# Optimization experiments

Measured on AMD Instinct MI355X. Metric: run time of the kernel, lower is better.

The kernel has to match this reference:

```python
import jax, jax.numpy as jnp
import numpy as np

DIM = 2048
N_HEADS = 16
N_KV_HEADS = 8
HEAD_DIM = DIM // N_HEADS  # 128
B, S = 4, 2048
EPS = 1e-6


def _xavier_uniform(key, shape):
    fan_out, fan_in = shape
    bound = float(np.sqrt(6.0 / (fan_in + fan_out)))
    return jax.random.uniform(key, shape, jnp.float32, -bound, bound)


def _rmsnorm(x, w):
    # x: [..., head_dim]
    return x * jax.lax.rsqrt(jnp.mean(x * x, axis=-1, keepdims=True) + EPS) * w


def _apply_rope(x, cos, sin):
    # x: [B,S,H,D]; cos/sin: [B,S,D//2]; pairs (even, odd) form complex numbers
    x2 = x.reshape(*x.shape[:-1], HEAD_DIM // 2, 2)
    xr, xi = x2[..., 0], x2[..., 1]
    c = cos[:, :, None, :]
    s = sin[:, :, None, :]
    out_r = xr * c - xi * s
    out_i = xr * s + xi * c
    return jnp.stack([out_r, out_i], axis=-1).reshape(x.shape)


def setup_inputs() -> dict:
    key = jax.random.key(0)
    k1, k2, k3 = jax.random.split(key, 3)
    x = jax.random.normal(k1, (B, S, DIM), jnp.float32)
    x_mask = jnp.ones((B, S), jnp.bool_)
    # rotary frequencies (llama-style)
    inv_freq = 1.0 / (10000.0 ** (np.arange(0, HEAD_DIM, 2, dtype=np.float32) / HEAD_DIM))
    angles = np.arange(S, dtype=np.float32)[:, None] * inv_freq[None, :]  # [S, D/2]
    freqs_cos = jnp.broadcast_to(jnp.asarray(np.cos(angles)), (B, S, HEAD_DIM // 2))
    freqs_sin = jnp.broadcast_to(jnp.asarray(np.sin(angles)), (B, S, HEAD_DIM // 2))
    qkv_out = (N_HEADS + 2 * N_KV_HEADS) * HEAD_DIM
    Wqkv = _xavier_uniform(k2, (qkv_out, DIM))
    Wout = _xavier_uniform(k3, (DIM, N_HEADS * HEAD_DIM))
    qn_w = jnp.ones((HEAD_DIM,), jnp.float32)
    kn_w = jnp.ones((HEAD_DIM,), jnp.float32)
    return {"x": x, "x_mask": x_mask, "freqs_cos": freqs_cos, "freqs_sin": freqs_sin,
            "Wqkv": Wqkv, "Wout": Wout, "qn_w": qn_w, "kn_w": kn_w}


def reference(x, x_mask, freqs_cos, freqs_sin, Wqkv, Wout, qn_w, kn_w):
    bsz, seqlen, _ = x.shape
    n_rep = N_HEADS // N_KV_HEADS
    qkv = x @ Wqkv.T  # [B,S,(H+2*KV)*D]
    q_sz = N_HEADS * HEAD_DIM
    kv_sz = N_KV_HEADS * HEAD_DIM
    xq = qkv[..., :q_sz].reshape(bsz, seqlen, N_HEADS, HEAD_DIM)
    xk = qkv[..., q_sz:q_sz + kv_sz].reshape(bsz, seqlen, N_KV_HEADS, HEAD_DIM)
    xv = qkv[..., q_sz + kv_sz:].reshape(bsz, seqlen, N_KV_HEADS, HEAD_DIM)
    xq = _rmsnorm(xq, qn_w)
    xk = _rmsnorm(xk, kn_w)
    xq = _apply_rope(xq, freqs_cos, freqs_sin)
    xk = _apply_rope(xk, freqs_cos, freqs_sin)
    # GQA: repeat kv heads contiguously (matches unsqueeze(3).repeat.flatten(2,3))
    xk = jnp.repeat(xk, n_rep, axis=2)  # [B,S,H,D]
    xv = jnp.repeat(xv, n_rep, axis=2)
    scale = float(np.sqrt(1.0 / HEAD_DIM))
    scores = jnp.einsum('bqhd,bkhd->bhqk', xq, xk) * scale  # [B,H,S,S]
    mask = x_mask[:, None, None, :]  # [B,1,1,S] key mask
    scores = jnp.where(mask, scores, jnp.asarray(-1e30, scores.dtype))
    attn = jax.nn.softmax(scores, axis=-1)
    out = jnp.einsum('bhqk,bkhd->bqhd', attn, xv)  # [B,S,H,D]
    out = out.reshape(bsz, seqlen, N_HEADS * HEAD_DIM)
    return out @ Wout.T
```

## Files before the change

### kernel.cpp

```cpp
#include <hip/hip_runtime.h>

typedef unsigned short u16;
typedef unsigned int   u32;
typedef __bf16  bf16x8 __attribute__((ext_vector_type(8)));
typedef float   f32x4  __attribute__((ext_vector_type(4)));
typedef u16     u16x8  __attribute__((ext_vector_type(8)));

#define DEV __device__ __forceinline__

DEV u16 f2bf(float f) {
  u32 u = __builtin_bit_cast(u32, f);
  u += 0x7fffu + ((u >> 16) & 1u);
  return (u16)(u >> 16);
}
DEV float bf2f(u16 h) { return __builtin_bit_cast(float, (u32)h << 16); }

DEV void gl2lds16(const void* g, void* l) {
  __builtin_amdgcn_global_load_lds(
      (const __attribute__((address_space(1))) u32*)g,
      (__attribute__((address_space(3))) u32*)l, 16, 0, 0);
}

DEV f32x4 mfma16(u16x8 a, u16x8 b, f32x4 c) {
  return __builtin_amdgcn_mfma_f32_16x16x32_bf16(
      __builtin_bit_cast(bf16x8, a), __builtin_bit_cast(bf16x8, b), c, 0, 0, 0);
}

__global__ __launch_bounds__(256) void k_cast(const float* __restrict__ in,
                                              u16* __restrict__ out, long n) {
  long i = ((long)blockIdx.x * 256 + threadIdx.x) * 8;
  if (i >= n) return;
  float4 a = *(const float4*)(in + i);
  float4 b = *(const float4*)(in + i + 4);
  u16x8 o;
  o[0]=f2bf(a.x); o[1]=f2bf(a.y); o[2]=f2bf(a.z); o[3]=f2bf(a.w);
  o[4]=f2bf(b.x); o[5]=f2bf(b.y); o[6]=f2bf(b.z); o[7]=f2bf(b.w);
  *(u16x8*)(out + i) = o;
}

template<bool F32OUT>
__global__ __launch_bounds__(512, 2) void k_gemm256(
    const u16* __restrict__ A, const u16* __restrict__ B,
    u16* __restrict__ Cb, float* __restrict__ Cf, int N, int K, int nbx)
{
  __shared__ __align__(16) u16 As2[2][16384];
  __shared__ __align__(16) u16 Bs2[2][16384];

  const int per = gridDim.x >> 3;
  const int wg  = (blockIdx.x & 7) * per + (blockIdx.x >> 3);
  const int by  = wg / nbx, bx = wg - by * nbx;
  const long m0 = (long)by * 256, n0 = (long)bx * 256;

  const int tid = threadIdx.x, wv = tid >> 6, lane = tid & 63;
  const int lr = lane & 15, lg = lane >> 4;
  const int wr = wv >> 2, wc = wv & 3;

  const int r8  = tid >> 3;
  const int u   = tid & 7;
  const int kux = ((u ^ (r8 & 7)) << 3);

  const int aoffb = wr * 8192 + lr * 64;
  const int boffb = (wc >> 1) * 8192 + (wc & 1) * 4096 + lr * 64;
  const int sw0 = ((lg ^ (lr & 7)) << 3);
  const int sw1 = (((4 + lg) ^ (lr & 7)) << 3);

  f32x4 acc[8][4] = {};

  auto stageK = [&](int d, int k0) {
#pragma unroll
    for (int h = 0; h < 2; ++h) {
      const u16* ga = A + (m0 + h * 128 + r8) * (long)K + k0 + kux;
      const u16* gb = B + (n0 + h * 128 + r8) * (long)K + k0 + kux;
      gl2lds16(ga,                 &As2[d][h * 8192 + tid * 8]);
      gl2lds16(ga + 64 * (long)K,  &As2[d][h * 8192 + 4096 + tid * 8]);
      gl2lds16(gb,                 &Bs2[d][h * 8192 + tid * 8]);
      gl2lds16(gb + 64 * (long)K,  &Bs2[d][h * 8192 + 4096 + tid * 8]);
    }
  };

  const int T = K >> 6;
  stageK(0, 0);
  stageK(1, 64);

  for (int t = 0; t < T; ++t) {
    const int d = t & 1;
    if (t < T - 1) asm volatile("s_waitcnt vmcnt(8)" ::: "memory");
    else           asm volatile("s_waitcnt vmcnt(0)" ::: "memory");
    asm volatile("s_barrier" ::: "memory");

#pragma unroll
    for (int kk = 0; kk < 2; ++kk) {
      const int sw = kk ? sw1 : sw0;
      u16x8 bfrag[4];
#pragma unroll
      for (int g = 0; g < 4; ++g)
        bfrag[g] = *(const u16x8*)(&Bs2[d][boffb + g * 1024 + sw]);
#pragma unroll
      for (int mh = 0; mh < 2; ++mh) {
        u16x8 afrag[4];
#pragma unroll
        for (int j = 0; j < 4; ++j)
          afrag[j] = *(const u16x8*)(&As2[d][aoffb + (mh * 4 + j) * 1024 + sw]);
        asm volatile("s_barrier" ::: "memory");
        __builtin_amdgcn_s_setprio(1);
#pragma unroll
        for (int j = 0; j < 4; ++j)
#pragma unroll
          for (int g = 0; g < 4; ++g)
            acc[mh * 4 + j][g] = mfma16(afrag[j], bfrag[g], acc[mh * 4 + j][g]);
        __builtin_amdgcn_s_setprio(0);
        asm volatile("s_barrier" ::: "memory");
      }
    }
    __builtin_amdgcn_sched_barrier(0);
    if (t + 2 < T) stageK(d, (t + 2) << 6);
  }

#pragma unroll
  for (int f = 0; f < 8; ++f)
#pragma unroll
    for (int g = 0; g < 4; ++g)
#pragma unroll
      for (int r = 0; r < 4; ++r) {
        long row = m0 + wr * 128 + f * 16 + lg * 4 + r;
        long col = n0 + wc * 64 + g * 16 + lr;
        if (F32OUT) Cf[row * N + col] = acc[f][g][r];
        else        Cb[row * N + col] = f2bf(acc[f][g][r]);
      }
}

__global__ __launch_bounds__(256) void k_normrope(
    const u16* __restrict__ qkv, const float* __restrict__ fc,
    const float* __restrict__ fs, const float* __restrict__ qn,
    const float* __restrict__ kn,
    u16* __restrict__ Qg, u16* __restrict__ Kg)
{
  const int m = blockIdx.x;
  const int b = m >> 11, s = m & 2047;
  const int wave = threadIdx.x >> 6, lane = threadIdx.x & 63;
  const u16* row = qkv + (long)m * 4096;
  const float c  = fc[(long)m * 64 + lane];
  const float sn = fs[(long)m * 64 + lane];
  const float w0q = qn[lane * 2], w1q = qn[lane * 2 + 1];
  const float w0k = kn[lane * 2], w1k = kn[lane * 2 + 1];
  const float QS = 0.12751744f;

  for (int slot = wave; slot < 24; slot += 4) {
    u32 pair = *(const u32*)(row + slot * 128 + lane * 2);
    float x0 = bf2f((u16)(pair & 0xffffu));
    float x1 = bf2f((u16)(pair >> 16));
    float ss = x0 * x0 + x1 * x1;
#pragma unroll
    for (int msk = 1; msk < 64; msk <<= 1) ss += __shfl_xor(ss, msk, 64);
    float rms = rsqrtf(ss * (1.0f / 128.0f) + 1e-6f);
    bool isq = slot < 16;
    float w0 = isq ? w0q : w0k;
    float w1 = isq ? w1q : w1k;
    float xr = x0 * rms * w0;
    float xi = x1 * rms * w1;
    float o0 = xr * c - xi * sn;
    float o1 = xr * sn + xi * c;
    if (isq) { o0 *= QS; o1 *= QS; }
    u32 outp = (u32)f2bf(o0) | ((u32)f2bf(o1) << 16);
    if (isq)
      *(u32*)(Qg + ((long)((b * 16 + slot) * 2048 + s)) * 128 + lane * 2) = outp;
    else
      *(u32*)(Kg + ((long)((b * 8 + slot - 16) * 2048 + s)) * 128 + lane * 2) = outp;
  }
}

__global__ __launch_bounds__(256) void k_vtrans(const u16* __restrict__ qkv,
                                                u16* __restrict__ Vt)
{
  __shared__ __align__(16) u16 Ls[128 * 128];
  const int st = blockIdx.x;
  const int bk = blockIdx.y;
  const int b = bk >> 3, kvh = bk & 7;
  const int t = threadIdx.x;
  const int s0 = st * 128;
  const u16* src = qkv + ((long)(b * 2048 + s0)) * 4096 + (24 + kvh) * 128;
#pragma unroll
  for (int i = 0; i < 8; ++i) {
    int gi = i * 2048 + t * 8;
    int sl = gi >> 7, d = gi & 127;
    u16x8 v = *(const u16x8*)(src + (long)sl * 4096 + d);
    int sw = ((sl ^ (sl >> 3)) & 7) << 3;
    *(u16x8*)(&Ls[sl * 128 + (d ^ sw)]) = v;
  }
  __syncthreads();
  u16* dst = Vt + ((long)bk * 128) * 2048 + s0;
#pragma unroll
  for (int i = 0; i < 8; ++i) {
    int d = i * 16 + (t >> 4);
    int sl0 = (t & 15) * 8;
    u16x8 o;
#pragma unroll
    for (int j = 0; j < 8; ++j) {
      int sl = sl0 + j;
      int sw = ((sl ^ (sl >> 3)) & 7) << 3;
      o[j] = Ls[sl * 128 + (d ^ sw)];
    }
    *(u16x8*)(dst + (long)d * 2048 + sl0) = o;
  }
}

__global__ __launch_bounds__(256, 2) void k_attn(
    const u16* __restrict__ Qg, const u16* __restrict__ Kg,
    const u16* __restrict__ Vt, u16* __restrict__ Og)
{
  __shared__ __align__(16) u16 Kl[2 * 64 * 128];
  __shared__ __align__(16) u16 Vl[2 * 128 * 64];
  __shared__ __align__(16) u16 Pl[4][32 * 32];

  const int f   = blockIdx.x;
  const int xcd = f & 7;
  const int s8  = f >> 3;
  const int b   = s8 >> 5;
  const int kvh = xcd;
  const int mem = s8 & 31;
  const int h   = kvh * 2 + (mem & 1);
  const int qblk= mem >> 1;

  const u16*  Qp = Qg + (long)(b * 16 + h) * 2048 * 128;
  const char* Kp = (const char*)(Kg + (long)(b * 8 + kvh) * 2048 * 128);
  const char* Vp = (const char*)(Vt + (long)(b * 8 + kvh) * 128 * 2048);

  const int tid = threadIdx.x, wave = tid >> 6, lane = tid & 63;
  const int lr = lane & 15, lg = lane >> 4;
  const int q0 = qblk * 128 + wave * 32;

  u16x8 qf[2][4];
#pragma unroll
  for (int ah = 0; ah < 2; ++ah)
#pragma unroll
    for (int kk = 0; kk < 4; ++kk)
      qf[ah][kk] = *(const u16x8*)(Qp + (long)(q0 + ah * 16 + lr) * 128 + kk * 32 + lg * 8);

  f32x4 oacc[2][8] = {};
  float lsum[2][4] = {};

  int koff[4], voff[4];
#pragma unroll
  for (int i = 0; i < 4; ++i) {
    int L = i * 4096 + tid * 16;
    int key = L >> 8;
    koff[i] = key * 256 + ((L & 255) ^ ((key & 7) << 4));
    int d = L >> 7;
    voff[i] = d * 4096 + ((L & 127) ^ ((d & 7) << 4));
  }
  char* Klb = (char*)Kl;
  char* Vlb = (char*)Vl;
  u16* Pw = &Pl[wave][0];

  auto stage = [&](int sel, int k0) {
#pragma unroll
    for (int i = 0; i < 4; ++i) {
      int L = i * 4096 + tid * 16;
      gl2lds16(Kp + (long)k0 * 256 + koff[i], Klb + sel * 16384 + L);
      gl2lds16(Vp + (long)k0 * 2   + voff[i], Vlb + sel * 16384 + L);
    }
  };

  stage(0, 0);

  int cur = 0;
  for (int t = 0; t < 32; ++t) {
    if (t < 31) {
      stage(cur ^ 1, (t + 1) * 64);
      asm volatile("s_waitcnt vmcnt(8)" ::: "memory");
    } else {
      asm volatile("s_waitcnt vmcnt(0)" ::: "memory");
    }
    asm volatile("s_barrier" ::: "memory");
    const u16* Kb = Kl + cur * 8192;
    const u16* Vb = Vl + cur * 8192;

#pragma unroll
    for (int h32 = 0; h32 < 2; ++h32) {
      f32x4 sf[2][2] = {};
      __builtin_amdgcn_s_setprio(1);
#pragma unroll
      for (int kk = 0; kk < 4; ++kk)
#pragma unroll
        for (int nt = 0; nt < 2; ++nt) {
          u16x8 kf = *(const u16x8*)(&Kb[(h32 * 32 + nt * 16 + lr) * 128 +
                                         ((kk * 32 + lg * 8) ^ ((lr & 7) << 3))]);
          sf[0][nt] = mfma16(qf[0][kk], kf, sf[0][nt]);
          sf[1][nt] = mfma16(qf[1][kk], kf, sf[1][nt]);
        }
      __builtin_amdgcn_s_setprio(0);
#pragma unroll
      for (int ah = 0; ah < 2; ++ah)
#pragma unroll
        for (int nt = 0; nt < 2; ++nt)
#pragma unroll
          for (int r = 0; r < 4; ++r) {
            float p = exp2f(sf[ah][nt][r]);
            u32 pb = __builtin_bit_cast(u32, p) >> 16;
            int q = ah * 16 + lg * 4 + r;
            Pw[q * 32 + ((nt * 16 + lr) ^ (lg << 3))] = (u16)pb;
            lsum[ah][r] += __builtin_bit_cast(float, pb << 16);
          }
      u16x8 pa[2];
#pragma unroll
      for (int ah = 0; ah < 2; ++ah)
        pa[ah] = *(const u16x8*)(&Pw[(ah * 16 + lr) * 32 +
                                     ((lg * 8) ^ (((lr >> 2) & 3) << 3))]);
      __builtin_amdgcn_s_setprio(1);
#pragma unroll
      for (int n = 0; n < 8; ++n) {
        u16x8 vb = *(const u16x8*)(&Vb[(n * 16 + lr) * 64 +
                                       ((h32 * 32 + lg * 8) ^ ((lr & 7) << 3))]);
        oacc[0][n] = mfma16(pa[0], vb, oacc[0][n]);
        oacc[1][n] = mfma16(pa[1], vb, oacc[1][n]);
      }
      __builtin_amdgcn_s_setprio(0);
    }

    asm volatile("s_barrier" ::: "memory");
    cur ^= 1;
  }

#pragma unroll
  for (int ah = 0; ah < 2; ++ah)
#pragma unroll
    for (int r = 0; r < 4; ++r) {
      float s = lsum[ah][r];
#pragma unroll
      for (int msk = 1; msk < 16; msk <<= 1) s += __shfl_xor(s, msk, 64);
      lsum[ah][r] = 1.0f / s;
    }

  const long sbase = (long)b * 2048 + q0;
#pragma unroll
  for (int ah = 0; ah < 2; ++ah)
#pragma unroll
    for (int n = 0; n < 8; ++n)
#pragma unroll
      for (int r = 0; r < 4; ++r) {
        long srow = sbase + ah * 16 + lg * 4 + r;
        Og[srow * 2048 + h * 128 + n * 16 + lr] = f2bf(oacc[ah][n][r] * lsum[ah][r]);
      }
}

extern "C" void kernel_launch(void* const* d_in, const int* in_sizes, int n_in,
                              void* d_out, int out_size, void* d_ws, size_t ws_size,
                              hipStream_t stream) {
  const float* x    = (const float*)d_in[0];
  const float* fc   = (const float*)d_in[2];
  const float* fs   = (const float*)d_in[3];
  const float* Wqkv = (const float*)d_in[4];
  const float* Wout = (const float*)d_in[5];
  const float* qn   = (const float*)d_in[6];
  const float* kn   = (const float*)d_in[7];
  float* out = (float*)d_out;

  const size_t XB_OFF   = 0;
  const size_t WQKV_OFF = 33554432;
  const size_t WOUT_OFF = 50331648;
  const size_t QKV_OFF  = 58720256;
  const size_t KG_OFF   = 125829120;
  const size_t VT_OFF   = 142606336;
  if (ws_size < 159383552) return;

  char* ws = (char*)d_ws;
  u16* xb    = (u16*)(ws + XB_OFF);
  u16* wqkvb = (u16*)(ws + WQKV_OFF);
  u16* woutb = (u16*)(ws + WOUT_OFF);
  u16* qkvb  = (u16*)(ws + QKV_OFF);
  u16* Qgb   = (u16*)(ws + XB_OFF);
  u16* Kgb   = (u16*)(ws + KG_OFF);
  u16* Vtb   = (u16*)(ws + VT_OFF);
  u16* Ogb   = (u16*)(ws + QKV_OFF);

  k_cast<<<8192, 256, 0, stream>>>(x,    xb,    16777216L);
  k_cast<<<4096, 256, 0, stream>>>(Wqkv, wqkvb, 8388608L);
  k_cast<<<2048, 256, 0, stream>>>(Wout, woutb, 4194304L);

  k_gemm256<false><<<512, 512, 0, stream>>>(xb, wqkvb, qkvb, nullptr, 4096, 2048, 16);

  k_vtrans<<<dim3(16, 32), 256, 0, stream>>>(qkvb, Vtb);
  k_normrope<<<8192, 256, 0, stream>>>(qkvb, fc, fs, qn, kn, Qgb, Kgb);

  k_attn<<<1024, 256, 0, stream>>>(Qgb, Kgb, Vtb, Ogb);

  k_gemm256<true><<<256, 512, 0, stream>>>(Ogb, woutb, nullptr, out, 2048, 2048, 8);
}
```

Before: 470.3 us.

## Double attention block to 8 waves and pack P as paired bf16 words

The attention kernel now uses 512-thread blocks covering 256 query rows. Each K/V tile staged in LDS is therefore shared by twice as many waves, and the launch grid is halved. The K-row mapping is interleaved so each lane's two score tiles land on adjacent keys. That lets the probabilities be packed two per 32-bit LDS store, with no XOR swizzle and half as many stores. Launch bounds now request 4 blocks per SM, which tightens register limits and could cause spills.

Result: slower. 928.2 us (+97.4%).

```diff
diff --git a/kernel.cpp b/kernel.cpp
--- a/kernel.cpp
+++ b/kernel.cpp
@@ -204,20 +204,20 @@
   }
 }
 
-__global__ __launch_bounds__(256, 2) void k_attn(
+__global__ __launch_bounds__(512, 4) void k_attn(
     const u16* __restrict__ Qg, const u16* __restrict__ Kg,
     const u16* __restrict__ Vt, u16* __restrict__ Og)
 {
   __shared__ __align__(16) u16 Kl[2 * 64 * 128];
   __shared__ __align__(16) u16 Vl[2 * 128 * 64];
-  __shared__ __align__(16) u16 Pl[4][32 * 32];
+  __shared__ __align__(16) u32 Pl[8][32 * 16];
 
   const int f   = blockIdx.x;
   const int xcd = f & 7;
-  const int s8  = f >> 3;
-  const int b   = s8 >> 5;
+  const int s6  = f >> 3;
+  const int b   = s6 >> 4;
   const int kvh = xcd;
-  const int mem = s8 & 31;
+  const int mem = s6 & 15;
   const int h   = kvh * 2 + (mem & 1);
   const int qblk= mem >> 1;
 
@@ -227,7 +227,7 @@
 
   const int tid = threadIdx.x, wave = tid >> 6, lane = tid & 63;
   const int lr = lane & 15, lg = lane >> 4;
-  const int q0 = qblk * 128 + wave * 32;
+  const int q0 = qblk * 256 + wave * 32;
 
   u16x8 qf[2][4];
 #pragma unroll
@@ -239,10 +239,10 @@
   f32x4 oacc[2][8] = {};
   float lsum[2][4] = {};
 
-  int koff[4], voff[4];
-#pragma unroll
-  for (int i = 0; i < 4; ++i) {
-    int L = i * 4096 + tid * 16;
+  int koff[2], voff[2];
+#pragma unroll
+  for (int i = 0; i < 2; ++i) {
+    int L = i * 8192 + tid * 16;
     int key = L >> 8;
     koff[i] = key * 256 + ((L & 255) ^ ((key & 7) << 4));
     int d = L >> 7;
@@ -250,12 +250,12 @@
   }
   char* Klb = (char*)Kl;
   char* Vlb = (char*)Vl;
-  u16* Pw = &Pl[wave][0];
+  u32* Pw = &Pl[wave][0];
 
   auto stage = [&](int sel, int k0) {
 #pragma unroll
-    for (int i = 0; i < 4; ++i) {
-      int L = i * 4096 + tid * 16;
+    for (int i = 0; i < 2; ++i) {
+      int L = i * 8192 + tid * 16;
       gl2lds16(Kp + (long)k0 * 256 + koff[i], Klb + sel * 16384 + L);
       gl2lds16(Vp + (long)k0 * 2   + voff[i], Vlb + sel * 16384 + L);
     }
@@ -267,7 +267,7 @@
   for (int t = 0; t < 32; ++t) {
     if (t < 31) {
       stage(cur ^ 1, (t + 1) * 64);
-      asm volatile("s_waitcnt vmcnt(8)" ::: "memory");
+      asm volatile("s_waitcnt vmcnt(4)" ::: "memory");
     } else {
       asm volatile("s_waitcnt vmcnt(0)" ::: "memory");
     }
@@ -283,8 +283,9 @@
       for (int kk = 0; kk < 4; ++kk)
 #pragma unroll
         for (int nt = 0; nt < 2; ++nt) {
-          u16x8 kf = *(const u16x8*)(&Kb[(h32 * 32 + nt * 16 + lr) * 128 +
-                                         ((kk * 32 + lg * 8) ^ ((lr & 7) << 3))]);
+          const int krow = h32 * 32 + 2 * lr + nt;
+          u16x8 kf = *(const u16x8*)(&Kb[krow * 128 +
+                                         ((kk * 32 + lg * 8) ^ ((krow & 7) << 3))]);
           sf[0][nt] = mfma16(qf[0][kk], kf, sf[0][nt]);
           sf[1][nt] = mfma16(qf[1][kk], kf, sf[1][nt]);
         }
@@ -292,20 +293,18 @@
 #pragma unroll
       for (int ah = 0; ah < 2; ++ah)
 #pragma unroll
-        for (int nt = 0; nt < 2; ++nt)
-#pragma unroll
-          for (int r = 0; r < 4; ++r) {
-            float p = exp2f(sf[ah][nt][r]);
-            u32 pb = __builtin_bit_cast(u32, p) >> 16;
-            int q = ah * 16 + lg * 4 + r;
-            Pw[q * 32 + ((nt * 16 + lr) ^ (lg << 3))] = (u16)pb;
-            lsum[ah][r] += __builtin_bit_cast(float, pb << 16);
-          }
+        for (int r = 0; r < 4; ++r) {
+          float p0 = exp2f(sf[ah][0][r]);
+          float p1 = exp2f(sf[ah][1][r]);
+          u32 pb0 = __builtin_bit_cast(u32, p0) >> 16;
+          u32 pb1 = __builtin_bit_cast(u32, p1) >> 16;
+          Pw[(ah * 16 + lg * 4 + r) * 16 + lr] = pb0 | (pb1 << 16);
+          lsum[ah][r] += bf2f((u16)pb0) + bf2f((u16)pb1);
+        }
       u16x8 pa[2];
 #pragma unroll
       for (int ah = 0; ah < 2; ++ah)
-        pa[ah] = *(const u16x8*)(&Pw[(ah * 16 + lr) * 32 +
-                                     ((lg * 8) ^ (((lr >> 2) & 3) << 3))]);
+        pa[ah] = *(const u16x8*)((const u16*)(Pw + (ah * 16 + lr) * 16 + lg * 4));
       __builtin_amdgcn_s_setprio(1);
 #pragma unroll
       for (int n = 0; n < 8; ++n) {
@@ -382,7 +381,7 @@
   k_vtrans<<<dim3(16, 32), 256, 0, stream>>>(qkvb, Vtb);
   k_normrope<<<8192, 256, 0, stream>>>(qkvb, fc, fs, qn, kn, Qgb, Kgb);
 
-  k_attn<<<1024, 256, 0, stream>>>(Qgb, Kgb, Vtb, Ogb);
+  k_attn<<<512, 512, 0, stream>>>(Qgb, Kgb, Vtb, Ogb);
 
   k_gemm256<true><<<256, 512, 0, stream>>>(Ogb, woutb, nullptr, out, 2048, 2048, 8);
 }
```
